# Kernel tuning notes

Measured on AMD Instinct MI355X. Metric: run time of the kernel, lower is better.

Reference implementation:

```python
import jax, jax.numpy as jnp
import numpy as np

B, S, H = 2, 2048, 2048
E, K = 8, 4
I_MOE, I_SH = 1408, 5632
NQ, NKV, DH = 16, 2, 128
EPS = 1e-5
ROPE_WL = 10000.0


def setup_inputs():
    key = jax.random.key(0)
    ks = jax.random.split(key, 18)
    f = lambda k, shp: jax.random.normal(k, shp, jnp.float32) * 0.02
    return {
        "decoder_sequence": jax.random.normal(ks[0], (B, S, H), jnp.float32),
        "ln1_scale": jnp.ones((H,), jnp.float32),
        "wq": f(ks[1], (H, NQ * DH)), "bq": f(ks[2], (NQ * DH,)),
        "wk": f(ks[3], (H, NKV * DH)), "bk": f(ks[4], (NKV * DH,)),
        "wv": f(ks[5], (H, NKV * DH)), "bv": f(ks[6], (NKV * DH,)),
        "wo": f(ks[7], (NQ * DH, H)),
        "ln2_scale": jnp.ones((H,), jnp.float32),
        "router_w": f(ks[8], (H, E)),
        "w_gate": f(ks[9], (E, H, I_MOE)),
        "w_up": f(ks[10], (E, H, I_MOE)),
        "w_down": f(ks[11], (E, I_MOE, H)),
        "sw_gate": f(ks[12], (H, I_SH)),
        "sw_up": f(ks[13], (H, I_SH)),
        "sw_down": f(ks[14], (I_SH, H)),
        "shared_gate_w": f(ks[15], (H, 1)),
    }


def _rms(x, scale):
    # QwenLayerNorm: RMSNorm in float32
    v = jnp.mean(jnp.square(x.astype(jnp.float32)), axis=-1, keepdims=True)
    return (x.astype(jnp.float32) * jax.lax.rsqrt(v + EPS) * scale).astype(x.dtype)


def _rope(x):
    # x: [B, S, heads, DH]; half-split rotary (keras-hub RotaryEmbedding)
    pos = jnp.arange(S, dtype=jnp.float32)
    inv = 1.0 / (ROPE_WL ** (jnp.arange(0, DH, 2, dtype=jnp.float32) / DH))
    ang = pos[:, None] * inv[None, :]                       # [S, DH/2]
    cos = jnp.cos(ang)[None, :, None, :]
    sin = jnp.sin(ang)[None, :, None, :]
    x1, x2 = jnp.split(x, 2, axis=-1)
    return jnp.concatenate([x1 * cos - x2 * sin, x2 * cos + x1 * sin], axis=-1)


def reference(decoder_sequence, ln1_scale, wq, bq, wk, bk, wv, bv, wo,
              ln2_scale, router_w, w_gate, w_up, w_down,
              sw_gate, sw_up, sw_down, shared_gate_w):
    x = decoder_sequence
    # --- self attention (pre-norm, causal, GQA, RoPE) ---
    h = _rms(x, ln1_scale)
    q = (h @ wq + bq).reshape(B, S, NQ, DH)
    k = (h @ wk + bk).reshape(B, S, NKV, DH)
    v = (h @ wv + bv).reshape(B, S, NKV, DH)
    q = _rope(q)
    k = _rope(k)
    rep = NQ // NKV
    k = jnp.repeat(k, rep, axis=2)
    v = jnp.repeat(v, rep, axis=2)
    scores = jnp.einsum('bqhd,bkhd->bhqk', q, k) / jnp.sqrt(jnp.float32(DH))
    causal = jnp.tril(jnp.ones((S, S), bool))
    scores = jnp.where(causal[None, None], scores, jnp.float32(-1e9))
    probs = jax.nn.softmax(scores, axis=-1)
    attn = jnp.einsum('bhqk,bkhd->bqhd', probs, v).reshape(B, S, NQ * DH)
    x = x + attn @ wo
    # --- sparse MoE block ---
    t = _rms(x, ln2_scale).reshape(B * S, H)
    router_logits = t @ router_w                             # [T, E]
    rw = jax.nn.softmax(router_logits, axis=-1)
    topw, topi = jax.lax.top_k(rw, K)
    topw = topw / jnp.sum(topw, axis=-1, keepdims=True)      # norm_topk_prob
    dense_w = jnp.zeros((B * S, E), t.dtype).at[
        jnp.arange(B * S)[:, None], topi].add(topw)          # [T, E]
    gate = jax.nn.silu(jnp.einsum('th,ehi->eti', t, w_gate))
    up = jnp.einsum('th,ehi->eti', t, w_up)
    eout = jnp.einsum('eti,eih->eth', gate * up, w_down)     # [E, T, H]
    moe = jnp.einsum('eth,te->th', eout, dense_w)
    # shared expert + sigmoid gate
    sh = (jax.nn.silu(t @ sw_gate) * (t @ sw_up)) @ sw_down
    sh = jax.nn.sigmoid(t @ shared_gate_w) * sh
    out = x + (moe + sh).reshape(B, S, H)
    return out
```

## Files before the change

kernel.cpp:

```cpp
#include <hip/hip_runtime.h>
#include <math.h>

static constexpr int BB   = 2;
static constexpr int SS   = 2048;
static constexpr int HH   = 2048;
static constexpr int TT   = BB * SS;
static constexpr int EE   = 8;
static constexpr int KSEL = 4;
static constexpr int IMOE = 1408;
static constexpr int ISH  = 5632;
static constexpr int NQ   = 16;
static constexpr int NKV  = 2;
static constexpr int DH   = 128;

typedef __attribute__((ext_vector_type(8))) short bhalf8;
typedef __attribute__((ext_vector_type(4))) float floatx4;

union U16B { uint4 u; bhalf8 s; };
__device__ __forceinline__ bhalf8 as_b8(uint4 u) { U16B x; x.u = u; return x.s; }

__device__ __forceinline__ void split_pack8(const float* f, uint4& hi, uint4& lo)
{
    unsigned h[4], lw[4];
#pragma unroll
    for (int q = 0; q < 4; ++q) {
        const float f0 = f[2 * q], f1 = f[2 * q + 1];
        const unsigned u0 = __float_as_uint(f0), u1 = __float_as_uint(f1);
        const unsigned m0 = u0 & 0xffff0000u, m1 = u1 & 0xffff0000u;
        h[q] = (u0 >> 16) | m1;
        const float l0 = f0 - __uint_as_float(m0);
        const float l1 = f1 - __uint_as_float(m1);
        lw[q] = (__float_as_uint(l0) >> 16) | (__float_as_uint(l1) & 0xffff0000u);
    }
    hi = make_uint4(h[0], h[1], h[2], h[3]);
    lo = make_uint4(lw[0], lw[1], lw[2], lw[3]);
}

__global__ __launch_bounds__(256)
void rmsnorm_k(const float* __restrict__ x, const float* __restrict__ sc,
               float* __restrict__ o)
{
    const int row = blockIdx.x;
    const float4* xr = (const float4*)(x + (size_t)row * HH);
    const float4* sr = (const float4*)sc;
    float4* orow = (float4*)(o + (size_t)row * HH);
    float ss = 0.f;
    for (int i = threadIdx.x; i < HH / 4; i += 256) {
        float4 v = xr[i];
        ss += v.x * v.x + v.y * v.y + v.z * v.z + v.w * v.w;
    }
#pragma unroll
    for (int off = 32; off > 0; off >>= 1) ss += __shfl_down(ss, off, 64);
    __shared__ float red[4];
    if ((threadIdx.x & 63) == 0) red[threadIdx.x >> 6] = ss;
    __syncthreads();
    const float tot = red[0] + red[1] + red[2] + red[3];
    const float inv = rsqrtf(tot / (float)HH + 1e-5f);
    for (int i = threadIdx.x; i < HH / 4; i += 256) {
        float4 v = xr[i]; float4 s = sr[i];
        float4 w;
        w.x = v.x * inv * s.x; w.y = v.y * inv * s.y;
        w.z = v.z * inv * s.z; w.w = v.w * inv * s.w;
        orow[i] = w;
    }
}

__global__ __launch_bounds__(256)
void zero_k(float* __restrict__ p, int n4)
{
    const int i = blockIdx.x * 256 + threadIdx.x;
    if (i < n4) ((float4*)p)[i] = make_float4(0.f, 0.f, 0.f, 0.f);
}

__global__ __launch_bounds__(256)
void gemm_k(const float* __restrict__ A, int lda,
            const float* __restrict__ Bm, int ldb,
            float* __restrict__ C, int ldc, int K,
            const float* __restrict__ bias,
            const float* __restrict__ rowscale,
            const float* __restrict__ add1,
            const float* __restrict__ add2,
            int accumulate,
            const int* __restrict__ arow,
            const int* __restrict__ crow,
            const int* __restrict__ mlim)
{
    const int m0 = blockIdx.y * 128;
    if (mlim && m0 >= *mlim) return;

    __shared__ uint4 lds[2048];
    uint4* Ahi = lds;
    uint4* Alo = lds + 512;
    uint4* Bhi = lds + 1024;
    uint4* Blo = lds + 1536;

    const int t  = threadIdx.x;
    const int n0 = blockIdx.x * 128;

    const int sar = t >> 1;
    const int sak = (t & 1) << 4;
    const int sbc = t & 127;
    const int sbk = (t >> 7) << 4;
    int arow_eff = m0 + sar;
    if (arow) { const int r = arow[arow_eff]; arow_eff = (r < 0) ? 0 : r; }
    const float* Ap = A + (size_t)arow_eff * lda + sak;
    const float* Bp = Bm + (size_t)sbk * ldb + n0 + sbc;
    const int aslot = ((sar >> 4) * 4 + (sak >> 3)) * 16 + (sar & 15);
    const int bslot = ((sbc >> 4) * 4 + (sbk >> 3)) * 16 + (sbc & 15);

    const int w  = t >> 6, l = t & 63;
    const int wr = w >> 1, wc = w & 1;
    const int lr = l & 15, kg = l >> 4;

    floatx4 acc[4][4];
#pragma unroll
    for (int i = 0; i < 4; ++i)
#pragma unroll
        for (int j = 0; j < 4; ++j) acc[i][j] = (floatx4){0.f, 0.f, 0.f, 0.f};

    float af[16], bf[16];
    *(float4*)&af[0]  = *(const float4*)(Ap + 0);
    *(float4*)&af[4]  = *(const float4*)(Ap + 4);
    *(float4*)&af[8]  = *(const float4*)(Ap + 8);
    *(float4*)&af[12] = *(const float4*)(Ap + 12);
#pragma unroll
    for (int j = 0; j < 16; ++j) bf[j] = Bp[(size_t)j * ldb];

    for (int k0 = 0; k0 < K; k0 += 32) {
        __syncthreads();
        {
            uint4 h0, l0, h1, l1;
            split_pack8(&af[0], h0, l0);
            split_pack8(&af[8], h1, l1);
            Ahi[aslot] = h0; Ahi[aslot + 16] = h1;
            Alo[aslot] = l0; Alo[aslot + 16] = l1;
            split_pack8(&bf[0], h0, l0);
            split_pack8(&bf[8], h1, l1);
            Bhi[bslot] = h0; Bhi[bslot + 16] = h1;
            Blo[bslot] = l0; Blo[bslot + 16] = l1;
        }
        __syncthreads();

        if (k0 + 32 < K) {
            const int kn = k0 + 32;
            *(float4*)&af[0]  = *(const float4*)(Ap + kn + 0);
            *(float4*)&af[4]  = *(const float4*)(Ap + kn + 4);
            *(float4*)&af[8]  = *(const float4*)(Ap + kn + 8);
            *(float4*)&af[12] = *(const float4*)(Ap + kn + 12);
#pragma unroll
            for (int j = 0; j < 16; ++j) bf[j] = Bp[(size_t)(kn + j) * ldb];
        }

        bhalf8 ah[4], al[4];
#pragma unroll
        for (int i = 0; i < 4; ++i) {
            const int s = ((wr * 4 + i) * 4 + kg) * 16 + lr;
            ah[i] = as_b8(Ahi[s]);
            al[i] = as_b8(Alo[s]);
        }
#pragma unroll
        for (int j = 0; j < 4; ++j) {
            const int s = ((wc * 4 + j) * 4 + kg) * 16 + lr;
            const bhalf8 bh = as_b8(Bhi[s]);
            const bhalf8 bl = as_b8(Blo[s]);
#pragma unroll
            for (int i = 0; i < 4; ++i) {
                acc[i][j] = __builtin_amdgcn_mfma_f32_16x16x32_bf16(ah[i], bl, acc[i][j], 0, 0, 0);
                acc[i][j] = __builtin_amdgcn_mfma_f32_16x16x32_bf16(al[i], bh, acc[i][j], 0, 0, 0);
                acc[i][j] = __builtin_amdgcn_mfma_f32_16x16x32_bf16(ah[i], bh, acc[i][j], 0, 0, 0);
            }
        }
    }

#pragma unroll
    for (int i = 0; i < 4; ++i) {
#pragma unroll
        for (int q = 0; q < 4; ++q) {
            const int m = m0 + (wr * 4 + i) * 16 + kg * 4 + q;
            int cm = m;
            if (crow) { cm = crow[m]; if (cm < 0) continue; }
            const float rs = rowscale ? rowscale[m] : 1.f;
#pragma unroll
            for (int j = 0; j < 4; ++j) {
                const int n = n0 + (wc * 4 + j) * 16 + lr;
                float v = acc[i][j][q];
                if (bias) v += bias[n];
                v *= rs;
                const size_t off = (size_t)cm * ldc + n;
                if (accumulate) v += C[off];
                if (add1) v += add1[off];
                if (add2) v += add2[off];
                C[off] = v;
            }
        }
    }
}

__global__ __launch_bounds__(256)
void rope_k(float* __restrict__ p, int nheads)
{
    const int idx = blockIdx.x * 256 + threadIdx.x;
    const int total = TT * nheads * (DH / 2);
    if (idx >= total) return;
    const int i  = idx & 63;
    const int hh = (idx >> 6) % nheads;
    const int tt = idx / (64 * nheads);
    const int s  = tt & (SS - 1);
    const float freq = expf(-(float)i * (9.210340371976184f / 64.f));
    const float ang = (float)s * freq;
    float sn, cs;
    sincosf(ang, &sn, &cs);
    float* base = p + ((size_t)tt * nheads + hh) * DH;
    const float x1 = base[i], x2 = base[i + 64];
    base[i]      = x1 * cs - x2 * sn;
    base[i + 64] = x2 * cs + x1 * sn;
}

static constexpr int QT   = 64;
static constexpr int KT   = 32;
static constexpr int QSTR = DH + 4;

__global__ __launch_bounds__(256)
void attn_k(const float* __restrict__ qb, const float* __restrict__ kb,
            const float* __restrict__ vb, float* __restrict__ ob)
{
    __shared__ float Qs[QT][QSTR];
    __shared__ float KVs[KT][QSTR];
    __shared__ float Ps[QT][KT + 1];
    __shared__ float Mrow[QT];
    __shared__ float Lrow[QT];

    const int t   = threadIdx.x;
    const int q0  = blockIdx.x * QT;
    const int hq  = blockIdx.y;
    const int bz  = blockIdx.z;
    const int kvh = hq >> 3;
    const float scl = 0.08838834764831845f;

    for (int i4 = t; i4 < QT * (DH / 4); i4 += 256) {
        const int qi = i4 >> 5, c4 = i4 & 31;
        float4 v = *((const float4*)(qb + ((size_t)(bz * SS + q0 + qi) * NQ + hq) * DH) + c4);
        v.x *= scl; v.y *= scl; v.z *= scl; v.w *= scl;
        *(float4*)&Qs[qi][c4 << 2] = v;
    }
    if (t < QT) { Mrow[t] = -1e30f; Lrow[t] = 0.f; }

    const int tr = t >> 4;
    const int tc = t & 15;
    float O[4][8] = {};

    const int nk = q0 + QT;
    for (int k0 = 0; k0 < nk; k0 += KT) {
        float4 kreg[4], vreg[4];
#pragma unroll
        for (int i = 0; i < 4; ++i) {
            const int idx4 = t + (i << 8);
            const int kj = idx4 >> 5, c4 = idx4 & 31;
            const size_t roff = ((size_t)(bz * SS + k0 + kj) * NKV + kvh) * DH + (c4 << 2);
            kreg[i] = *(const float4*)(kb + roff);
            vreg[i] = *(const float4*)(vb + roff);
        }
        __syncthreads();
#pragma unroll
        for (int i = 0; i < 4; ++i) {
            const int idx4 = t + (i << 8);
            *(float4*)&KVs[idx4 >> 5][(idx4 & 31) << 2] = kreg[i];
        }
        __syncthreads();

        float s0[4] = {}, s1[4] = {};
#pragma unroll 8
        for (int d = 0; d < DH; d += 4) {
            const float4 ka = *(const float4*)&KVs[tc][d];
            const float4 kb4 = *(const float4*)&KVs[tc + 16][d];
#pragma unroll
            for (int i = 0; i < 4; ++i) {
                const float4 qv = *(const float4*)&Qs[(tr << 2) + i][d];
                s0[i] += qv.x * ka.x + qv.y * ka.y + qv.z * ka.z + qv.w * ka.w;
                s1[i] += qv.x * kb4.x + qv.y * kb4.y + qv.z * kb4.z + qv.w * kb4.w;
            }
        }

#pragma unroll
        for (int i = 0; i < 4; ++i) {
            const int qg = q0 + (tr << 2) + i;
            const float a  = (k0 + tc      <= qg) ? s0[i] : -1e30f;
            const float bq_ = (k0 + tc + 16 <= qg) ? s1[i] : -1e30f;
            float mt = fmaxf(a, bq_);
#pragma unroll
            for (int o = 1; o < 16; o <<= 1) mt = fmaxf(mt, __shfl_xor(mt, o, 64));
            const float mold = Mrow[(tr << 2) + i];
            const float mnew = fmaxf(mold, mt);
            const float alpha = __expf(mold - mnew);
            const float p0 = __expf(a - mnew);
            const float p1 = __expf(bq_ - mnew);
            float ls = p0 + p1;
#pragma unroll
            for (int o = 1; o < 16; o <<= 1) ls += __shfl_xor(ls, o, 64);
            if (tc == 0) {
                Mrow[(tr << 2) + i] = mnew;
                Lrow[(tr << 2) + i] = alpha * Lrow[(tr << 2) + i] + ls;
            }
            Ps[(tr << 2) + i][tc]      = p0;
            Ps[(tr << 2) + i][tc + 16] = p1;
#pragma unroll
            for (int j = 0; j < 8; ++j) O[i][j] *= alpha;
        }
        __syncthreads();
#pragma unroll
        for (int i = 0; i < 4; ++i) {
            const int idx4 = t + (i << 8);
            *(float4*)&KVs[idx4 >> 5][(idx4 & 31) << 2] = vreg[i];
        }
        __syncthreads();

#pragma unroll 4
        for (int kj = 0; kj < KT; ++kj) {
            const float4 v0 = *(const float4*)&KVs[kj][tc << 2];
            const float4 v1 = *(const float4*)&KVs[kj][64 + (tc << 2)];
#pragma unroll
            for (int i = 0; i < 4; ++i) {
                const float p = Ps[(tr << 2) + i][kj];
                O[i][0] += p * v0.x; O[i][1] += p * v0.y;
                O[i][2] += p * v0.z; O[i][3] += p * v0.w;
                O[i][4] += p * v1.x; O[i][5] += p * v1.y;
                O[i][6] += p * v1.z; O[i][7] += p * v1.w;
            }
        }
    }

#pragma unroll
    for (int i = 0; i < 4; ++i) {
        const int qi = (tr << 2) + i;
        const float inv = 1.f / Lrow[qi];
        float* base = ob + ((size_t)(bz * SS + q0 + qi) * NQ + hq) * DH;
        float4 o0, o1;
        o0.x = O[i][0] * inv; o0.y = O[i][1] * inv; o0.z = O[i][2] * inv; o0.w = O[i][3] * inv;
        o1.x = O[i][4] * inv; o1.y = O[i][5] * inv; o1.z = O[i][6] * inv; o1.w = O[i][7] * inv;
        *(float4*)(base + (tc << 2)) = o0;
        *(float4*)(base + 64 + (tc << 2)) = o1;
    }
}

__global__ __launch_bounds__(256)
void router_k(const float* __restrict__ tb, const float* __restrict__ rw,
              const float* __restrict__ sgw, float* __restrict__ dw,
              float* __restrict__ gs)
{
    const int tok = blockIdx.x;
    const float* xr = tb + (size_t)tok * HH;
    float acc[EE] = {};
    float ag = 0.f;
    for (int h = threadIdx.x; h < HH; h += 256) {
        const float xv = xr[h];
        const float4 r0 = *(const float4*)(rw + (size_t)h * EE);
        const float4 r1 = *(const float4*)(rw + (size_t)h * EE + 4);
        acc[0] += xv * r0.x; acc[1] += xv * r0.y; acc[2] += xv * r0.z; acc[3] += xv * r0.w;
        acc[4] += xv * r1.x; acc[5] += xv * r1.y; acc[6] += xv * r1.z; acc[7] += xv * r1.w;
        ag += xv * sgw[h];
    }
#pragma unroll
    for (int e = 0; e < EE; ++e)
#pragma unroll
        for (int o = 32; o > 0; o >>= 1) acc[e] += __shfl_down(acc[e], o, 64);
#pragma unroll
    for (int o = 32; o > 0; o >>= 1) ag += __shfl_down(ag, o, 64);
    __shared__ float red[4][EE + 1];
    if ((threadIdx.x & 63) == 0) {
        const int w = threadIdx.x >> 6;
#pragma unroll
        for (int e = 0; e < EE; ++e) red[w][e] = acc[e];
        red[w][EE] = ag;
    }
    __syncthreads();
    if (threadIdx.x == 0) {
        float l[EE];
#pragma unroll
        for (int e = 0; e < EE; ++e) l[e] = red[0][e] + red[1][e] + red[2][e] + red[3][e];
        const float g = red[0][EE] + red[1][EE] + red[2][EE] + red[3][EE];
        gs[tok] = 1.f / (1.f + expf(-g));
        float m = l[0];
        for (int e = 1; e < EE; ++e) m = fmaxf(m, l[e]);
        float p[EE]; float sum = 0.f;
        for (int e = 0; e < EE; ++e) { p[e] = expf(l[e] - m); sum += p[e]; }
        for (int e = 0; e < EE; ++e) p[e] /= sum;
        bool used[EE] = {};
        float wsum = 0.f;
        for (int k = 0; k < KSEL; ++k) {
            int bi = 0; float bv = -1.f;
            for (int e = 0; e < EE; ++e)
                if (!used[e] && p[e] > bv) { bv = p[e]; bi = e; }
            used[bi] = true; wsum += bv;
        }
        for (int e = 0; e < EE; ++e)
            dw[(size_t)tok * EE + e] = used[e] ? p[e] / wsum : 0.f;
    }
}

__global__ void route_init_k(int* __restrict__ cnt)
{
    if (threadIdx.x < EE) cnt[threadIdx.x] = 0;
}

__global__ __launch_bounds__(256)
void route_fill_k(const float* __restrict__ dw, int* __restrict__ cnt,
                  int* __restrict__ tokidx, float* __restrict__ tokw)
{
    const int t = blockIdx.x * 256 + threadIdx.x;
    if (t >= TT) return;
#pragma unroll
    for (int e = 0; e < EE; ++e) {
        const float w = dw[(size_t)t * EE + e];
        if (w > 0.f) {
            const int pos = atomicAdd(cnt + e, 1);
            tokidx[e * TT + pos] = t;
            tokw[e * TT + pos]   = w;
        }
    }
}

__global__ void route_pad_k(const int* __restrict__ cnt, int* __restrict__ mpad,
                            int* __restrict__ tokidx)
{
    const int e = blockIdx.x;
    const int c = cnt[e];
    const int mp = (c + 127) & ~127;
    if (threadIdx.x == 0) mpad[e] = mp;
    for (int i = c + threadIdx.x; i < mp; i += 64) tokidx[e * TT + i] = -1;
}

__global__ __launch_bounds__(256)
void silu_mul_k(float* __restrict__ g, const float* __restrict__ u,
                const float* __restrict__ dw, int ecol, int icols, int n,
                const int* __restrict__ mlim)
{
    const int idx = blockIdx.x * 256 + threadIdx.x;
    if (idx >= n) return;
    if (mlim && idx >= (*mlim) * icols) return;
    const float gv = g[idx];
    const float uv = u[idx];
    float v = gv / (1.f + __expf(-gv)) * uv;
    if (dw) v *= dw[(size_t)(idx / icols) * EE + ecol];
    g[idx] = v;
}

extern "C" void kernel_launch(void* const* d_in, const int* in_sizes, int n_in,
                              void* d_out, int out_size, void* d_ws, size_t ws_size,
                              hipStream_t stream)
{
    (void)in_sizes; (void)n_in; (void)out_size;
    const float* x   = (const float*)d_in[0];
    const float* ln1 = (const float*)d_in[1];
    const float* wq  = (const float*)d_in[2];
    const float* bq  = (const float*)d_in[3];
    const float* wk  = (const float*)d_in[4];
    const float* bk  = (const float*)d_in[5];
    const float* wv  = (const float*)d_in[6];
    const float* bv  = (const float*)d_in[7];
    const float* wo  = (const float*)d_in[8];
    const float* ln2 = (const float*)d_in[9];
    const float* rww = (const float*)d_in[10];
    const float* wg  = (const float*)d_in[11];
    const float* wu  = (const float*)d_in[12];
    const float* wd  = (const float*)d_in[13];
    const float* swg = (const float*)d_in[14];
    const float* swu = (const float*)d_in[15];
    const float* swd = (const float*)d_in[16];
    const float* sgw = (const float*)d_in[17];
    float* out = (float*)d_out;

    float* ws   = (float*)d_ws;
    float* hbuf = ws;
    float* qb   = hbuf + (size_t)TT * HH;
    float* kb   = qb   + (size_t)TT * NQ * DH;
    float* vb   = kb   + (size_t)TT * NKV * DH;
    float* x1   = vb   + (size_t)TT * NKV * DH;
    float* moe  = x1   + (size_t)TT * HH;
    float* gbuf = moe  + (size_t)TT * HH;
    float* ubuf = gbuf + (size_t)TT * IMOE;
    float* dw   = ubuf + (size_t)TT * IMOE;
    float* gs   = dw   + (size_t)TT * EE;
    int*   tokidx = (int*)(gs + TT);
    float* tokw   = (float*)(tokidx + (size_t)EE * TT);
    int*   cnt    = (int*)(tokw + (size_t)EE * TT);
    int*   mpad   = cnt + EE;
    const size_t need_bytes = (size_t)((char*)(mpad + EE) - (char*)ws);
    if (ws_size < need_bytes) return;

    float* attnb = hbuf;
    float* tb    = qb;

    rmsnorm_k<<<TT, 256, 0, stream>>>(x, ln1, hbuf);
    gemm_k<<<dim3((NQ * DH) / 128, TT / 128), 256, 0, stream>>>(hbuf, HH, wq, NQ * DH, qb, NQ * DH, HH, bq, nullptr, nullptr, nullptr, 0, nullptr, nullptr, nullptr);
    gemm_k<<<dim3((NKV * DH) / 128, TT / 128), 256, 0, stream>>>(hbuf, HH, wk, NKV * DH, kb, NKV * DH, HH, bk, nullptr, nullptr, nullptr, 0, nullptr, nullptr, nullptr);
    gemm_k<<<dim3((NKV * DH) / 128, TT / 128), 256, 0, stream>>>(hbuf, HH, wv, NKV * DH, vb, NKV * DH, HH, bv, nullptr, nullptr, nullptr, 0, nullptr, nullptr, nullptr);
    rope_k<<<(TT * NQ * 64 + 255) / 256, 256, 0, stream>>>(qb, NQ);
    rope_k<<<(TT * NKV * 64 + 255) / 256, 256, 0, stream>>>(kb, NKV);
    attn_k<<<dim3(SS / QT, NQ, BB), 256, 0, stream>>>(qb, kb, vb, attnb);
    gemm_k<<<dim3(HH / 128, TT / 128), 256, 0, stream>>>(attnb, NQ * DH, wo, HH, x1, HH, NQ * DH, nullptr, nullptr, x, nullptr, 0, nullptr, nullptr, nullptr);
    rmsnorm_k<<<TT, 256, 0, stream>>>(x1, ln2, tb);
    router_k<<<TT, 256, 0, stream>>>(tb, rww, sgw, dw, gs);
    zero_k<<<(TT * HH / 4 + 255) / 256, 256, 0, stream>>>(moe, TT * HH / 4);
    route_init_k<<<1, 64, 0, stream>>>(cnt);
    route_fill_k<<<(TT + 255) / 256, 256, 0, stream>>>(dw, cnt, tokidx, tokw);
    route_pad_k<<<EE, 64, 0, stream>>>(cnt, mpad, tokidx);
    const int nmoe = TT * IMOE;
    for (int e = 0; e < EE; ++e) {
        const float* wge = wg + (size_t)e * HH * IMOE;
        const float* wue = wu + (size_t)e * HH * IMOE;
        const float* wde = wd + (size_t)e * IMOE * HH;
        const int*   idx = tokidx + e * TT;
        const float* twe = tokw + e * TT;
        const int*   ml  = mpad + e;
        gemm_k<<<dim3(IMOE / 128, TT / 128), 256, 0, stream>>>(tb, HH, wge, IMOE, gbuf, IMOE, HH, nullptr, nullptr, nullptr, nullptr, 0, idx, nullptr, ml);
        gemm_k<<<dim3(IMOE / 128, TT / 128), 256, 0, stream>>>(tb, HH, wue, IMOE, ubuf, IMOE, HH, nullptr, nullptr, nullptr, nullptr, 0, idx, nullptr, ml);
        silu_mul_k<<<(nmoe + 255) / 256, 256, 0, stream>>>(gbuf, ubuf, nullptr, 0, IMOE, nmoe, ml);
        gemm_k<<<dim3(HH / 128, TT / 128), 256, 0, stream>>>(gbuf, IMOE, wde, HH, moe, HH, IMOE, nullptr, twe, nullptr, nullptr, 1, nullptr, idx, ml);
    }
    for (int c = 0; c < 4; ++c) {
        const float* swgc = swg + (size_t)c * IMOE;
        const float* swuc = swu + (size_t)c * IMOE;
        const float* swdc = swd + (size_t)c * IMOE * HH;
        gemm_k<<<dim3(IMOE / 128, TT / 128), 256, 0, stream>>>(tb, HH, swgc, ISH, gbuf, IMOE, HH, nullptr, nullptr, nullptr, nullptr, 0, nullptr, nullptr, nullptr);
        gemm_k<<<dim3(IMOE / 128, TT / 128), 256, 0, stream>>>(tb, HH, swuc, ISH, ubuf, IMOE, HH, nullptr, nullptr, nullptr, nullptr, 0, nullptr, nullptr, nullptr);
        silu_mul_k<<<(nmoe + 255) / 256, 256, 0, stream>>>(gbuf, ubuf, nullptr, 0, IMOE, nmoe, nullptr);
        if (c < 3)
            gemm_k<<<dim3(HH / 128, TT / 128), 256, 0, stream>>>(gbuf, IMOE, swdc, HH, moe, HH, IMOE, nullptr, gs, nullptr, nullptr, 1, nullptr, nullptr, nullptr);
        else
            gemm_k<<<dim3(HH / 128, TT / 128), 256, 0, stream>>>(gbuf, IMOE, swdc, HH, out, HH, IMOE, nullptr, gs, moe, x1, 0, nullptr, nullptr, nullptr);
    }
}
```

Measured before the change: 5.921 ms.

## Pre-split weights into transposed bf16 hi/lo planes for GEMM B operand

Adds a splitw_k pass that transposes every weight matrix and splits it into bf16 high and low planes in workspace. A new gemm_p_k then loads these planes directly instead of loading fp32 B and doing the split and pack inside the inner loop. This removes per-tile conversion work and halves B-side bytes per plane load. In exchange, every call pays an extra pass that reads all weights and writes twice as many 16-bit values, and it needs a large workspace, falling back to the old path when the workspace is too small.

```diff
diff --git a/kernel.cpp b/kernel.cpp
--- a/kernel.cpp
+++ b/kernel.cpp
@@ -73,17 +73,175 @@
 }
 
 __global__ __launch_bounds__(256)
-void gemm_k(const float* __restrict__ A, int lda,
-            const float* __restrict__ Bm, int ldb,
-            float* __restrict__ C, int ldc, int K,
-            const float* __restrict__ bias,
-            const float* __restrict__ rowscale,
-            const float* __restrict__ add1,
-            const float* __restrict__ add2,
-            int accumulate,
-            const int* __restrict__ arow,
-            const int* __restrict__ crow,
-            const int* __restrict__ mlim)
+void splitw_k(const float* __restrict__ W, int K, int N,
+              unsigned short* __restrict__ th, unsigned short* __restrict__ tl)
+{
+    const size_t zoff = (size_t)blockIdx.z * K * N;
+    W += zoff; th += zoff; tl += zoff;
+    __shared__ float tile[64][65];
+    const int k0 = blockIdx.y * 64;
+    const int n0 = blockIdx.x * 64;
+    const int t  = threadIdx.x;
+    const int c  = t & 63, rq = t >> 6;
+#pragma unroll
+    for (int r = 0; r < 16; ++r) {
+        const int kk = r * 4 + rq;
+        tile[kk][c] = W[(size_t)(k0 + kk) * N + n0 + c];
+    }
+    __syncthreads();
+#pragma unroll
+    for (int r = 0; r < 16; ++r) {
+        const int nn = r * 4 + rq;
+        const float v = tile[c][nn];
+        const unsigned u  = __float_as_uint(v);
+        const unsigned hm = u & 0xffff0000u;
+        const float lo = v - __uint_as_float(hm);
+        th[(size_t)(n0 + nn) * K + k0 + c] = (unsigned short)(u >> 16);
+        tl[(size_t)(n0 + nn) * K + k0 + c] = (unsigned short)(__float_as_uint(lo) >> 16);
+    }
+}
+
+__global__ __launch_bounds__(256)
+void gemm_p_k(const float* __restrict__ A, int lda,
+              const unsigned short* __restrict__ Bth,
+              const unsigned short* __restrict__ Btl, int ldbt,
+              float* __restrict__ C, int ldc, int K,
+              const float* __restrict__ bias,
+              const float* __restrict__ rowscale,
+              const float* __restrict__ add1,
+              const float* __restrict__ add2,
+              int accumulate,
+              const int* __restrict__ arow,
+              const int* __restrict__ crow,
+              const int* __restrict__ mlim)
+{
+    const int m0 = blockIdx.y * 128;
+    if (mlim && m0 >= *mlim) return;
+
+    __shared__ uint4 lds[2048];
+    uint4* Ahi = lds;
+    uint4* Alo = lds + 512;
+    uint4* Bhi = lds + 1024;
+    uint4* Blo = lds + 1536;
+
+    const int t  = threadIdx.x;
+    const int n0 = blockIdx.x * 128;
+
+    const int sar = t >> 1;
+    const int sak = (t & 1) << 4;
+    const int sbc = t & 127;
+    const int sbk = (t >> 7) << 4;
+    int arow_eff = m0 + sar;
+    if (arow) { const int r = arow[arow_eff]; arow_eff = (r < 0) ? 0 : r; }
+    const float* Ap = A + (size_t)arow_eff * lda + sak;
+    const unsigned short* Bph = Bth + (size_t)(n0 + sbc) * ldbt + sbk;
+    const unsigned short* Bpl = Btl + (size_t)(n0 + sbc) * ldbt + sbk;
+    const int aslot = ((sar >> 4) * 4 + (sak >> 3)) * 16 + (sar & 15);
+    const int bslot = ((sbc >> 4) * 4 + (sbk >> 3)) * 16 + (sbc & 15);
+
+    const int w  = t >> 6, l = t & 63;
+    const int wr = w >> 1, wc = w & 1;
+    const int lr = l & 15, kg = l >> 4;
+
+    floatx4 acc[4][4];
+#pragma unroll
+    for (int i = 0; i < 4; ++i)
+#pragma unroll
+        for (int j = 0; j < 4; ++j) acc[i][j] = (floatx4){0.f, 0.f, 0.f, 0.f};
+
+    float af[16];
+    uint4 rbh0, rbh1, rbl0, rbl1;
+    *(float4*)&af[0]  = *(const float4*)(Ap + 0);
+    *(float4*)&af[4]  = *(const float4*)(Ap + 4);
+    *(float4*)&af[8]  = *(const float4*)(Ap + 8);
+    *(float4*)&af[12] = *(const float4*)(Ap + 12);
+    rbh0 = *(const uint4*)(Bph);
+    rbh1 = *(const uint4*)(Bph + 8);
+    rbl0 = *(const uint4*)(Bpl);
+    rbl1 = *(const uint4*)(Bpl + 8);
+
+    for (int k0 = 0; k0 < K; k0 += 32) {
+        __syncthreads();
+        {
+            uint4 h0, l0, h1, l1;
+            split_pack8(&af[0], h0, l0);
+            split_pack8(&af[8], h1, l1);
+            Ahi[aslot] = h0; Ahi[aslot + 16] = h1;
+            Alo[aslot] = l0; Alo[aslot + 16] = l1;
+            Bhi[bslot] = rbh0; Bhi[bslot + 16] = rbh1;
+            Blo[bslot] = rbl0; Blo[bslot + 16] = rbl1;
+        }
+        __syncthreads();
+
+        if (k0 + 32 < K) {
+            const int kn = k0 + 32;
+            *(float4*)&af[0]  = *(const float4*)(Ap + kn + 0);
+            *(float4*)&af[4]  = *(const float4*)(Ap + kn + 4);
+            *(float4*)&af[8]  = *(const float4*)(Ap + kn + 8);
+            *(float4*)&af[12] = *(const float4*)(Ap + kn + 12);
+            rbh0 = *(const uint4*)(Bph + kn);
+            rbh1 = *(const uint4*)(Bph + kn + 8);
+            rbl0 = *(const uint4*)(Bpl + kn);
+            rbl1 = *(const uint4*)(Bpl + kn + 8);
+        }
+
+        bhalf8 ah[4], al[4];
+#pragma unroll
+        for (int i = 0; i < 4; ++i) {
+            const int s = ((wr * 4 + i) * 4 + kg) * 16 + lr;
+            ah[i] = as_b8(Ahi[s]);
+            al[i] = as_b8(Alo[s]);
+        }
+#pragma unroll
+        for (int j = 0; j < 4; ++j) {
+            const int s = ((wc * 4 + j) * 4 + kg) * 16 + lr;
+            const bhalf8 bh = as_b8(Bhi[s]);
+            const bhalf8 bl = as_b8(Blo[s]);
+#pragma unroll
+            for (int i = 0; i < 4; ++i) {
+                acc[i][j] = __builtin_amdgcn_mfma_f32_16x16x32_bf16(ah[i], bl, acc[i][j], 0, 0, 0);
+                acc[i][j] = __builtin_amdgcn_mfma_f32_16x16x32_bf16(al[i], bh, acc[i][j], 0, 0, 0);
+                acc[i][j] = __builtin_amdgcn_mfma_f32_16x16x32_bf16(ah[i], bh, acc[i][j], 0, 0, 0);
+            }
+        }
+    }
+
+#pragma unroll
+    for (int i = 0; i < 4; ++i) {
+#pragma unroll
+        for (int q = 0; q < 4; ++q) {
+            const int m = m0 + (wr * 4 + i) * 16 + kg * 4 + q;
+            int cm = m;
+            if (crow) { cm = crow[m]; if (cm < 0) continue; }
+            const float rs = rowscale ? rowscale[m] : 1.f;
+#pragma unroll
+            for (int j = 0; j < 4; ++j) {
+                const int n = n0 + (wc * 4 + j) * 16 + lr;
+                float v = acc[i][j][q];
+                if (bias) v += bias[n];
+                v *= rs;
+                const size_t off = (size_t)cm * ldc + n;
+                if (accumulate) v += C[off];
+                if (add1) v += add1[off];
+                if (add2) v += add2[off];
+                C[off] = v;
+            }
+        }
+    }
+}
+
+__global__ __launch_bounds__(256)
+void gemm_f_k(const float* __restrict__ A, int lda,
+              const float* __restrict__ Bm, int ldb,
+              float* __restrict__ C, int ldc, int K,
+              const float* __restrict__ bias,
+              const float* __restrict__ rowscale,
+              const float* __restrict__ add1,
+              const float* __restrict__ add2,
+              int accumulate,
+              const int* __restrict__ arow,
+              const int* __restrict__ crow,
+              const int* __restrict__ mlim)
 {
     const int m0 = blockIdx.y * 128;
     if (mlim && m0 >= *mlim) return;
@@ -484,20 +642,68 @@
     float* tokw   = (float*)(tokidx + (size_t)EE * TT);
     int*   cnt    = (int*)(tokw + (size_t)EE * TT);
     int*   mpad   = cnt + EE;
-    const size_t need_bytes = (size_t)((char*)(mpad + EE) - (char*)ws);
-    if (ws_size < need_bytes) return;
+    const size_t need_f32 = (size_t)((char*)(mpad + EE) - (char*)ws);
+    if (ws_size < need_f32) return;
+
+    char* pc0 = (char*)(mpad + EE);
+    pc0 = (char*)(((uintptr_t)pc0 + 15) & ~(uintptr_t)15);
+    unsigned short* p = (unsigned short*)pc0;
+    unsigned short* wq_th = p; p += (size_t)HH * (NQ * DH);
+    unsigned short* wq_tl = p; p += (size_t)HH * (NQ * DH);
+    unsigned short* wk_th = p; p += (size_t)HH * (NKV * DH);
+    unsigned short* wk_tl = p; p += (size_t)HH * (NKV * DH);
+    unsigned short* wv_th = p; p += (size_t)HH * (NKV * DH);
+    unsigned short* wv_tl = p; p += (size_t)HH * (NKV * DH);
+    unsigned short* wo_th = p; p += (size_t)HH * HH;
+    unsigned short* wo_tl = p; p += (size_t)HH * HH;
+    unsigned short* wg_th = p; p += (size_t)EE * HH * IMOE;
+    unsigned short* wg_tl = p; p += (size_t)EE * HH * IMOE;
+    unsigned short* wu_th = p; p += (size_t)EE * HH * IMOE;
+    unsigned short* wu_tl = p; p += (size_t)EE * HH * IMOE;
+    unsigned short* wd_th = p; p += (size_t)EE * IMOE * HH;
+    unsigned short* wd_tl = p; p += (size_t)EE * IMOE * HH;
+    unsigned short* sg_th = p; p += (size_t)HH * ISH;
+    unsigned short* sg_tl = p; p += (size_t)HH * ISH;
+    unsigned short* su_th = p; p += (size_t)HH * ISH;
+    unsigned short* su_tl = p; p += (size_t)HH * ISH;
+    unsigned short* sd_th = p; p += (size_t)ISH * HH;
+    unsigned short* sd_tl = p; p += (size_t)ISH * HH;
+    const size_t need_planes = (size_t)((char*)p - (char*)ws);
+    const bool planes = (ws_size >= need_planes);
 
     float* attnb = hbuf;
     float* tb    = qb;
 
+    if (planes) {
+        splitw_k<<<dim3((NQ * DH) / 64, HH / 64), 256, 0, stream>>>(wq, HH, NQ * DH, wq_th, wq_tl);
+        splitw_k<<<dim3((NKV * DH) / 64, HH / 64), 256, 0, stream>>>(wk, HH, NKV * DH, wk_th, wk_tl);
+        splitw_k<<<dim3((NKV * DH) / 64, HH / 64), 256, 0, stream>>>(wv, HH, NKV * DH, wv_th, wv_tl);
+        splitw_k<<<dim3(HH / 64, HH / 64), 256, 0, stream>>>(wo, NQ * DH, HH, wo_th, wo_tl);
+        splitw_k<<<dim3(IMOE / 64, HH / 64, EE), 256, 0, stream>>>(wg, HH, IMOE, wg_th, wg_tl);
+        splitw_k<<<dim3(IMOE / 64, HH / 64, EE), 256, 0, stream>>>(wu, HH, IMOE, wu_th, wu_tl);
+        splitw_k<<<dim3(HH / 64, IMOE / 64, EE), 256, 0, stream>>>(wd, IMOE, HH, wd_th, wd_tl);
+        splitw_k<<<dim3(ISH / 64, HH / 64), 256, 0, stream>>>(swg, HH, ISH, sg_th, sg_tl);
+        splitw_k<<<dim3(ISH / 64, HH / 64), 256, 0, stream>>>(swu, HH, ISH, su_th, su_tl);
+        splitw_k<<<dim3(HH / 64, ISH / 64), 256, 0, stream>>>(swd, ISH, HH, sd_th, sd_tl);
+    }
+
     rmsnorm_k<<<TT, 256, 0, stream>>>(x, ln1, hbuf);
-    gemm_k<<<dim3((NQ * DH) / 128, TT / 128), 256, 0, stream>>>(hbuf, HH, wq, NQ * DH, qb, NQ * DH, HH, bq, nullptr, nullptr, nullptr, 0, nullptr, nullptr, nullptr);
-    gemm_k<<<dim3((NKV * DH) / 128, TT / 128), 256, 0, stream>>>(hbuf, HH, wk, NKV * DH, kb, NKV * DH, HH, bk, nullptr, nullptr, nullptr, 0, nullptr, nullptr, nullptr);
-    gemm_k<<<dim3((NKV * DH) / 128, TT / 128), 256, 0, stream>>>(hbuf, HH, wv, NKV * DH, vb, NKV * DH, HH, bv, nullptr, nullptr, nullptr, 0, nullptr, nullptr, nullptr);
+    if (planes) {
+        gemm_p_k<<<dim3((NQ * DH) / 128, TT / 128), 256, 0, stream>>>(hbuf, HH, wq_th, wq_tl, HH, qb, NQ * DH, HH, bq, nullptr, nullptr, nullptr, 0, nullptr, nullptr, nullptr);
+        gemm_p_k<<<dim3((NKV * DH) / 128, TT / 128), 256, 0, stream>>>(hbuf, HH, wk_th, wk_tl, HH, kb, NKV * DH, HH, bk, nullptr, nullptr, nullptr, 0, nullptr, nullptr, nullptr);
+        gemm_p_k<<<dim3((NKV * DH) / 128, TT / 128), 256, 0, stream>>>(hbuf, HH, wv_th, wv_tl, HH, vb, NKV * DH, HH, bv, nullptr, nullptr, nullptr, 0, nullptr, nullptr, nullptr);
+    } else {
+        gemm_f_k<<<dim3((NQ * DH) / 128, TT / 128), 256, 0, stream>>>(hbuf, HH, wq, NQ * DH, qb, NQ * DH, HH, bq, nullptr, nullptr, nullptr, 0, nullptr, nullptr, nullptr);
+        gemm_f_k<<<dim3((NKV * DH) / 128, TT / 128), 256, 0, stream>>>(hbuf, HH, wk, NKV * DH, kb, NKV * DH, HH, bk, nullptr, nullptr, nullptr, 0, nullptr, nullptr, nullptr);
+        gemm_f_k<<<dim3((NKV * DH) / 128, TT / 128), 256, 0, stream>>>(hbuf, HH, wv, NKV * DH, vb, NKV * DH, HH, bv, nullptr, nullptr, nullptr, 0, nullptr, nullptr, nullptr);
+    }
     rope_k<<<(TT * NQ * 64 + 255) / 256, 256, 0, stream>>>(qb, NQ);
     rope_k<<<(TT * NKV * 64 + 255) / 256, 256, 0, stream>>>(kb, NKV);
     attn_k<<<dim3(SS / QT, NQ, BB), 256, 0, stream>>>(qb, kb, vb, attnb);
-    gemm_k<<<dim3(HH / 128, TT / 128), 256, 0, stream>>>(attnb, NQ * DH, wo, HH, x1, HH, NQ * DH, nullptr, nullptr, x, nullptr, 0, nullptr, nullptr, nullptr);
+    if (planes)
+        gemm_p_k<<<dim3(HH / 128, TT / 128), 256, 0, stream>>>(attnb, NQ * DH, wo_th, wo_tl, NQ * DH, x1, HH, NQ * DH, nullptr, nullptr, x, nullptr, 0, nullptr, nullptr, nullptr);
+    else
+        gemm_f_k<<<dim3(HH / 128, TT / 128), 256, 0, stream>>>(attnb, NQ * DH, wo, HH, x1, HH, NQ * DH, nullptr, nullptr, x, nullptr, 0, nullptr, nullptr, nullptr);
     rmsnorm_k<<<TT, 256, 0, stream>>>(x1, ln2, tb);
     router_k<<<TT, 256, 0, stream>>>(tb, rww, sgw, dw, gs);
     zero_k<<<(TT * HH / 4 + 255) / 256, 256, 0, stream>>>(moe, TT * HH / 4);
@@ -506,27 +712,44 @@
     route_pad_k<<<EE, 64, 0, stream>>>(cnt, mpad, tokidx);
     const int nmoe = TT * IMOE;
     for (int e = 0; e < EE; ++e) {
-        const float* wge = wg + (size_t)e * HH * IMOE;
-        const float* wue = wu + (size_t)e * HH * IMOE;
-        const float* wde = wd + (size_t)e * IMOE * HH;
         const int*   idx = tokidx + e * TT;
         const float* twe = tokw + e * TT;
         const int*   ml  = mpad + e;
-        gemm_k<<<dim3(IMOE / 128, TT / 128), 256, 0, stream>>>(tb, HH, wge, IMOE, gbuf, IMOE, HH, nullptr, nullptr, nullptr, nullptr, 0, idx, nullptr, ml);
-        gemm_k<<<dim3(IMOE / 128, TT / 128), 256, 0, stream>>>(tb, HH, wue, IMOE, ubuf, IMOE, HH, nullptr, nullptr, nullptr, nullptr, 0, idx, nullptr, ml);
-        silu_mul_k<<<(nmoe + 255) / 256, 256, 0, stream>>>(gbuf, ubuf, nullptr, 0, IMOE, nmoe, ml);
-        gemm_k<<<dim3(HH / 128, TT / 128), 256, 0, stream>>>(gbuf, IMOE, wde, HH, moe, HH, IMOE, nullptr, twe, nullptr, nullptr, 1, nullptr, idx, ml);
+        if (planes) {
+            gemm_p_k<<<dim3(IMOE / 128, TT / 128), 256, 0, stream>>>(tb, HH, wg_th + (size_t)e * HH * IMOE, wg_tl + (size_t)e * HH * IMOE, HH, gbuf, IMOE, HH, nullptr, nullptr, nullptr, nullptr, 0, idx, nullptr, ml);
+            gemm_p_k<<<dim3(IMOE / 128, TT / 128), 256, 0, stream>>>(tb, HH, wu_th + (size_t)e * HH * IMOE, wu_tl + (size_t)e * HH * IMOE, HH, ubuf, IMOE, HH, nullptr, nullptr, nullptr, nullptr, 0, idx, nullptr, ml);
+            silu_mul_k<<<(nmoe + 255) / 256, 256, 0, stream>>>(gbuf, ubuf, nullptr, 0, IMOE, nmoe, ml);
+            gemm_p_k<<<dim3(HH / 128, TT / 128), 256, 0, stream>>>(gbuf, IMOE, wd_th + (size_t)e * IMOE * HH, wd_tl + (size_t)e * IMOE * HH, IMOE, moe, HH, IMOE, nullptr, twe, nullptr, nullptr, 1, nullptr, idx, ml);
+        } else {
+            const float* wge = wg + (size_t)e * HH * IMOE;
+            const float* wue = wu + (size_t)e * HH * IMOE;
+            const float* wde = wd + (size_t)e * IMOE * HH;
+            gemm_f_k<<<dim3(IMOE / 128, TT / 128), 256, 0, stream>>>(tb, HH, wge, IMOE, gbuf, IMOE, HH, nullptr, nullptr, nullptr, nullptr, 0, idx, nullptr, ml);
+            gemm_f_k<<<dim3(IMOE / 128, TT / 128), 256, 0, stream>>>(tb, HH, wue, IMOE, ubuf, IMOE, HH, nullptr, nullptr, nullptr, nullptr, 0, idx, nullptr, ml);
+            silu_mul_k<<<(nmoe + 255) / 256, 256, 0, stream>>>(gbuf, ubuf, nullptr, 0, IMOE, nmoe, ml);
+            gemm_f_k<<<dim3(HH / 128, TT / 128), 256, 0, stream>>>(gbuf, IMOE, wde, HH, moe, HH, IMOE, nullptr, twe, nullptr, nullptr, 1, nullptr, idx, ml);
+        }
     }
     for (int c = 0; c < 4; ++c) {
-        const float* swgc = swg + (size_t)c * IMOE;
-        const float* swuc = swu + (size_t)c * IMOE;
-        const float* swdc = swd + (size_t)c * IMOE * HH;
-        gemm_k<<<dim3(IMOE / 128, TT / 128), 256, 0, stream>>>(tb, HH, swgc, ISH, gbuf, IMOE, HH, nullptr, nullptr, nullptr, nullptr, 0, nullptr, nullptr, nullptr);
-        gemm_k<<<dim3(IMOE / 128, TT / 128), 256, 0, stream>>>(tb, HH, swuc, ISH, ubuf, IMOE, HH, nullptr, nullptr, nullptr, nullptr, 0, nullptr, nullptr, nullptr);
-        silu_mul_k<<<(nmoe + 255) / 256, 256, 0, stream>>>(gbuf, ubuf, nullptr, 0, IMOE, nmoe, nullptr);
-        if (c < 3)
-            gemm_k<<<dim3(HH / 128, TT / 128), 256, 0, stream>>>(gbuf, IMOE, swdc, HH, moe, HH, IMOE, nullptr, gs, nullptr, nullptr, 1, nullptr, nullptr, nullptr);
-        else
-            gemm_k<<<dim3(HH / 128, TT / 128), 256, 0, stream>>>(gbuf, IMOE, swdc, HH, out, HH, IMOE, nullptr, gs, moe, x1, 0, nullptr, nullptr, nullptr);
-    }
-}
+        if (planes) {
+            gemm_p_k<<<dim3(IMOE / 128, TT / 128), 256, 0, stream>>>(tb, HH, sg_th + (size_t)c * IMOE * HH, sg_tl + (size_t)c * IMOE * HH, HH, gbuf, IMOE, HH, nullptr, nullptr, nullptr, nullptr, 0, nullptr, nullptr, nullptr);
+            gemm_p_k<<<dim3(IMOE / 128, TT / 128), 256, 0, stream>>>(tb, HH, su_th + (size_t)c * IMOE * HH, su_tl + (size_t)c * IMOE * HH, HH, ubuf, IMOE, HH, nullptr, nullptr, nullptr, nullptr, 0, nullptr, nullptr, nullptr);
+            silu_mul_k<<<(nmoe + 255) / 256, 256, 0, stream>>>(gbuf, ubuf, nullptr, 0, IMOE, nmoe, nullptr);
+            if (c < 3)
+                gemm_p_k<<<dim3(HH / 128, TT / 128), 256, 0, stream>>>(gbuf, IMOE, sd_th + (size_t)c * IMOE, sd_tl + (size_t)c * IMOE, ISH, moe, HH, IMOE, nullptr, gs, nullptr, nullptr, 1, nullptr, nullptr, nullptr);
+            else
+                gemm_p_k<<<dim3(HH / 128, TT / 128), 256, 0, stream>>>(gbuf, IMOE, sd_th + (size_t)c * IMOE, sd_tl + (size_t)c * IMOE, ISH, out, HH, IMOE, nullptr, gs, moe, x1, 0, nullptr, nullptr, nullptr);
+        } else {
+            const float* swgc = swg + (size_t)c * IMOE;
+            const float* swuc = swu + (size_t)c * IMOE;
+            const float* swdc = swd + (size_t)c * IMOE * HH;
+            gemm_f_k<<<dim3(IMOE / 128, TT / 128), 256, 0, stream>>>(tb, HH, swgc, ISH, gbuf, IMOE, HH, nullptr, nullptr, nullptr, nullptr, 0, nullptr, nullptr, nullptr);
+            gemm_f_k<<<dim3(IMOE / 128, TT / 128), 256, 0, stream>>>(tb, HH, swuc, ISH, ubuf, IMOE, HH, nullptr, nullptr, nullptr, nullptr, 0, nullptr, nullptr, nullptr);
+            silu_mul_k<<<(nmoe + 255) / 256, 256, 0, stream>>>(gbuf, ubuf, nullptr, 0, IMOE, nmoe, nullptr);
+            if (c < 3)
+                gemm_f_k<<<dim3(HH / 128, TT / 128), 256, 0, stream>>>(gbuf, IMOE, swdc, HH, moe, HH, IMOE, nullptr, gs, nullptr, nullptr, 1, nullptr, nullptr, nullptr);
+            else
+                gemm_f_k<<<dim3(HH / 128, TT / 128), 256, 0, stream>>>(gbuf, IMOE, swdc, HH, out, HH, IMOE, nullptr, gs, moe, x1, 0, nullptr, nullptr, nullptr);
+        }
+    }
+}
```

Measured after the change: 5.905 ms. No clear change (-0.3%).
